# Optimization experiments

Hardware: AMD Instinct MI355X
Metric: run time of the kernel (lower is better)

## Reference

```python
import jax, jax.numpy as jnp
import numpy as np

B, S, H = 2, 2048, 3072
NH, NKV, HD = 32, 8, 96
ROPE_THETA = 10000.0
NEG = -1e9


def setup_inputs() -> dict:
    key = jax.random.key(0)
    k0, k1, k2 = jax.random.split(key, 3)
    hidden_states = jax.random.normal(k0, (B, S, H), jnp.float32) * 0.02
    # rotary embeddings (precomputed, as HF passes position_embeddings=(cos,sin))
    inv_freq = 1.0 / (ROPE_THETA ** (jnp.arange(0, HD, 2, dtype=jnp.float32) / HD))
    pos = jnp.arange(S, dtype=jnp.float32)
    freqs = pos[:, None] * inv_freq[None, :]            # [S, HD/2]
    emb = jnp.concatenate([freqs, freqs], axis=-1)      # [S, HD]
    cos = jnp.broadcast_to(jnp.cos(emb)[None], (B, S, HD))
    sin = jnp.broadcast_to(jnp.sin(emb)[None], (B, S, HD))
    # additive causal mask [B,1,S,S]
    causal = jnp.tril(jnp.ones((S, S), dtype=bool))
    attention_mask = jnp.where(causal, 0.0, NEG).astype(jnp.float32)
    attention_mask = jnp.broadcast_to(attention_mask[None, None], (B, 1, S, S))
    Wqkv = jax.random.normal(k1, ((NH + 2 * NKV) * HD, H), jnp.float32) * 0.02
    Wo = jax.random.normal(k2, (H, NH * HD), jnp.float32) * 0.02
    cache_position = jnp.arange(S, dtype=jnp.int32)
    position_ids = jnp.broadcast_to(jnp.arange(S, dtype=jnp.int32)[None], (B, S))
    return {"hidden_states": hidden_states, "cos": cos, "sin": sin,
            "attention_mask": attention_mask, "Wqkv": Wqkv, "Wo": Wo,
            "cache_position": cache_position, "position_ids": position_ids}


def _rotate_half(x):
    x1, x2 = x[..., : HD // 2], x[..., HD // 2:]
    return jnp.concatenate([-x2, x1], axis=-1)


def reference(hidden_states, cos, sin, attention_mask, Wqkv, Wo, cache_position, position_ids):
    # fused qkv projection (no bias in Phi3)
    qkv = jnp.einsum('bsh,dh->bsd', hidden_states, Wqkv)  # [B,S,(NH+2*NKV)*HD]
    q = qkv[..., : NH * HD].reshape(B, S, NH, HD).transpose(0, 2, 1, 3)           # [B,NH,S,HD]
    k = qkv[..., NH * HD: (NH + NKV) * HD].reshape(B, S, NKV, HD).transpose(0, 2, 1, 3)
    v = qkv[..., (NH + NKV) * HD:].reshape(B, S, NKV, HD).transpose(0, 2, 1, 3)   # [B,NKV,S,HD]
    # rotary embedding (unsqueeze head dim)
    cosb, sinb = cos[:, None], sin[:, None]              # [B,1,S,HD]
    q = q * cosb + _rotate_half(q) * sinb
    k = k * cosb + _rotate_half(k) * sinb
    # DynamicCache() is empty -> cache update is identity (k, v unchanged)
    # GQA: repeat kv heads
    rep = NH // NKV
    k = jnp.repeat(k, rep, axis=1)                       # [B,NH,S,HD]
    v = jnp.repeat(v, rep, axis=1)
    # SDPA
    scale = 1.0 / jnp.sqrt(jnp.float32(HD))
    scores = jnp.einsum('bhqd,bhkd->bhqk', q, k) * scale + attention_mask
    attn = jax.nn.softmax(scores, axis=-1)
    ctx = jnp.einsum('bhqk,bhkd->bhqd', attn, v)         # [B,NH,S,HD]
    ctx = ctx.transpose(0, 2, 1, 3).reshape(B, S, NH * HD)
    out = jnp.einsum('bsd,hd->bsh', ctx, Wo)             # o_proj
    return out
```

## Files before the change

### kernel.cpp

```cpp
#include <hip/hip_runtime.h>

typedef __attribute__((ext_vector_type(8))) __bf16 bf16x8;
typedef __attribute__((ext_vector_type(4))) float f32x4;
typedef __attribute__((ext_vector_type(4))) unsigned int u32x4;
typedef __attribute__((ext_vector_type(4))) unsigned short u16x4;
typedef __attribute__((ext_vector_type(8))) unsigned short u16x8;

__device__ __forceinline__ unsigned short f2bf(float x) {
  unsigned u = __builtin_bit_cast(unsigned, x);
  u += 0x7fffu + ((u >> 16) & 1u);
  return (unsigned short)(u >> 16);
}
__device__ __forceinline__ float bf2f(unsigned short h) {
  unsigned u = ((unsigned)h) << 16;
  return __builtin_bit_cast(float, u);
}
__device__ __forceinline__ bf16x8 ld_frag(const unsigned short* p) {
  u32x4 u = *(const u32x4*)p;
  return __builtin_bit_cast(bf16x8, u);
}
__device__ __forceinline__ void gload_lds16(const unsigned short* g, unsigned short* l) {
  __builtin_amdgcn_global_load_lds(
      (const __attribute__((address_space(1))) void*)g,
      (__attribute__((address_space(3))) void*)l, 16, 0, 0);
}

__global__ __launch_bounds__(256) void cvt_bf16(const float* __restrict__ in,
                                                unsigned short* __restrict__ out, int n4) {
  int i = blockIdx.x * 256 + threadIdx.x;
  if (i >= n4) return;
  f32x4 v = *((const f32x4*)in + i);
  u16x4 o;
  #pragma unroll
  for (int j = 0; j < 4; ++j) o[j] = f2bf(v[j]);
  *((u16x4*)out + i) = o;
}

template <int WRITE_BF16>
__global__ __launch_bounds__(512, 2) void gemm8p(const unsigned short* __restrict__ A,
                                                 const unsigned short* __restrict__ B,
                                                 void* __restrict__ Cv,
                                                 int M, int N, int K) {
  __shared__ __align__(16) unsigned short SM[57344];
  const int nwg = gridDim.x;
  const int swz = (blockIdx.x & 7) * (nwg >> 3) + (blockIdx.x >> 3);
  const int bx = swz & 15, by = swz >> 4;
  const int row0 = bx * 256, col0 = by * 192;
  const int tid = threadIdx.x;
  const int wave = tid >> 6, lane = tid & 63;
  const int g = lane >> 4, r = lane & 15;
  const int wm = (wave >> 2) * 128, wn = (wave & 3) * 48;
  const int NT = K >> 6;

  const unsigned short* Agb = A + (size_t)row0 * K;
  const unsigned short* Bgb = B + (size_t)col0 * K;

  f32x4 acc[8][3] = {};

  auto SU = [&](const unsigned short* src, unsigned short* dst, int u) {
    const int pos = u * 512 + tid;
    const int rw = pos >> 3, cc = pos & 7;
    gload_lds16(src + (size_t)rw * K + ((cc ^ (rw & 7)) * 8), dst + pos * 8);
  };
  auto LDA = [&](const unsigned short* base, int mi, int dk) {
    const int rw = wm + mi * 16 + r;
    return ld_frag(base + rw * 64 + (((dk * 4 + g) ^ (r & 7)) * 8));
  };
  auto LDB = [&](const unsigned short* base, int ni, int dk) {
    const int rw = wn + ni * 16 + r;
    return ld_frag(base + rw * 64 + (((dk * 4 + g) ^ (r & 7)) * 8));
  };

  SU(Agb, SM, 0); SU(Agb, SM, 1); SU(Agb, SM, 2); SU(Agb, SM, 3);
  SU(Bgb, SM + 16384, 0); SU(Bgb, SM + 16384, 1); SU(Bgb, SM + 16384, 2);
  __syncthreads();

  for (int t = 0; t < NT; ++t) {
    const int d = t & 1;
    const unsigned short* Ab = SM + d * 28672;
    const unsigned short* Bb = Ab + 16384;
    unsigned short* An = SM + (d ^ 1) * 28672;
    unsigned short* Bn = An + 16384;
    const unsigned short* Asrc = Agb + (t + 1) * 64;
    const unsigned short* Bsrc = Bgb + (t + 1) * 64;
    const bool pf = (t + 1 < NT);

    bf16x8 a[4], b0, b1, b2;

    b0 = LDB(Bb, 0, 0); b1 = LDB(Bb, 1, 0); b2 = LDB(Bb, 2, 0);
    a[0] = LDA(Ab, 0, 0); a[1] = LDA(Ab, 1, 0); a[2] = LDA(Ab, 2, 0); a[3] = LDA(Ab, 3, 0);
    if (pf) { SU(Asrc, An, 0); SU(Asrc, An, 1); SU(Asrc, An, 2); }
    __builtin_amdgcn_s_barrier();
    asm volatile("s_waitcnt lgkmcnt(0)" ::: "memory");
    __builtin_amdgcn_sched_barrier(0);
    __builtin_amdgcn_s_setprio(1);
    #pragma unroll
    for (int i = 0; i < 4; ++i) {
      acc[i][0] = __builtin_amdgcn_mfma_f32_16x16x32_bf16(a[i], b0, acc[i][0], 0, 0, 0);
      acc[i][1] = __builtin_amdgcn_mfma_f32_16x16x32_bf16(a[i], b1, acc[i][1], 0, 0, 0);
      acc[i][2] = __builtin_amdgcn_mfma_f32_16x16x32_bf16(a[i], b2, acc[i][2], 0, 0, 0);
    }
    __builtin_amdgcn_s_setprio(0);
    __builtin_amdgcn_s_barrier();

    a[0] = LDA(Ab, 4, 0); a[1] = LDA(Ab, 5, 0); a[2] = LDA(Ab, 6, 0); a[3] = LDA(Ab, 7, 0);
    if (pf) { SU(Asrc, An, 3); SU(Bsrc, Bn, 0); }
    __builtin_amdgcn_s_barrier();
    asm volatile("s_waitcnt lgkmcnt(0)" ::: "memory");
    __builtin_amdgcn_sched_barrier(0);
    __builtin_amdgcn_s_setprio(1);
    #pragma unroll
    for (int i = 0; i < 4; ++i) {
      acc[4 + i][0] = __builtin_amdgcn_mfma_f32_16x16x32_bf16(a[i], b0, acc[4 + i][0], 0, 0, 0);
      acc[4 + i][1] = __builtin_amdgcn_mfma_f32_16x16x32_bf16(a[i], b1, acc[4 + i][1], 0, 0, 0);
      acc[4 + i][2] = __builtin_amdgcn_mfma_f32_16x16x32_bf16(a[i], b2, acc[4 + i][2], 0, 0, 0);
    }
    __builtin_amdgcn_s_setprio(0);
    __builtin_amdgcn_s_barrier();

    b0 = LDB(Bb, 0, 1); b1 = LDB(Bb, 1, 1); b2 = LDB(Bb, 2, 1);
    a[0] = LDA(Ab, 0, 1); a[1] = LDA(Ab, 1, 1); a[2] = LDA(Ab, 2, 1); a[3] = LDA(Ab, 3, 1);
    if (pf) { SU(Bsrc, Bn, 1); SU(Bsrc, Bn, 2); }
    __builtin_amdgcn_s_barrier();
    asm volatile("s_waitcnt lgkmcnt(0)" ::: "memory");
    __builtin_amdgcn_sched_barrier(0);
    __builtin_amdgcn_s_setprio(1);
    #pragma unroll
    for (int i = 0; i < 4; ++i) {
      acc[i][0] = __builtin_amdgcn_mfma_f32_16x16x32_bf16(a[i], b0, acc[i][0], 0, 0, 0);
      acc[i][1] = __builtin_amdgcn_mfma_f32_16x16x32_bf16(a[i], b1, acc[i][1], 0, 0, 0);
      acc[i][2] = __builtin_amdgcn_mfma_f32_16x16x32_bf16(a[i], b2, acc[i][2], 0, 0, 0);
    }
    __builtin_amdgcn_s_setprio(0);
    __builtin_amdgcn_s_barrier();

    a[0] = LDA(Ab, 4, 1); a[1] = LDA(Ab, 5, 1); a[2] = LDA(Ab, 6, 1); a[3] = LDA(Ab, 7, 1);
    __builtin_amdgcn_s_barrier();
    asm volatile("s_waitcnt lgkmcnt(0)" ::: "memory");
    __builtin_amdgcn_sched_barrier(0);
    __builtin_amdgcn_s_setprio(1);
    #pragma unroll
    for (int i = 0; i < 4; ++i) {
      acc[4 + i][0] = __builtin_amdgcn_mfma_f32_16x16x32_bf16(a[i], b0, acc[4 + i][0], 0, 0, 0);
      acc[4 + i][1] = __builtin_amdgcn_mfma_f32_16x16x32_bf16(a[i], b1, acc[4 + i][1], 0, 0, 0);
      acc[4 + i][2] = __builtin_amdgcn_mfma_f32_16x16x32_bf16(a[i], b2, acc[4 + i][2], 0, 0, 0);
    }
    __builtin_amdgcn_s_setprio(0);
    asm volatile("s_waitcnt vmcnt(0)" ::: "memory");
    __builtin_amdgcn_s_barrier();
  }

  #pragma unroll
  for (int mi = 0; mi < 8; ++mi)
    #pragma unroll
    for (int n = 0; n < 3; ++n)
      #pragma unroll
      for (int rr = 0; rr < 4; ++rr) {
        const size_t idx = (size_t)(row0 + wm + mi * 16 + g * 4 + rr) * (size_t)N
                         + (col0 + wn + n * 16 + r);
        if (WRITE_BF16) ((unsigned short*)Cv)[idx] = f2bf(acc[mi][n][rr]);
        else            ((float*)Cv)[idx] = acc[mi][n][rr];
      }
}

__global__ __launch_bounds__(256) void rope_qk(unsigned short* __restrict__ qkv,
                                               const float* __restrict__ cs,
                                               const float* __restrict__ sn) {
  const int t = blockIdx.x * 256 + threadIdx.x;
  const int d4 = t % 12;
  const int rest = t / 12;
  const int head = rest % 40;
  const int row = rest / 40;
  const size_t base = (size_t)row * 4608 + head * 96 + d4 * 4;
  const u16x4 a = *(const u16x4*)&qkv[base];
  const u16x4 bq = *(const u16x4*)&qkv[base + 48];
  const int cb = row * 96 + d4 * 4;
  const f32x4 c1 = *(const f32x4*)&cs[cb];
  const f32x4 s1 = *(const f32x4*)&sn[cb];
  const f32x4 c2 = *(const f32x4*)&cs[cb + 48];
  const f32x4 s2 = *(const f32x4*)&sn[cb + 48];
  u16x4 o1, o2;
  #pragma unroll
  for (int j = 0; j < 4; ++j) {
    const float x1 = bf2f(a[j]), x2 = bf2f(bq[j]);
    o1[j] = f2bf(x1 * c1[j] - x2 * s1[j]);
    o2[j] = f2bf(x2 * c2[j] + x1 * s2[j]);
  }
  *(u16x4*)&qkv[base] = o1;
  *(u16x4*)&qkv[base + 48] = o2;
}

__global__ __launch_bounds__(256) void vtrans(const unsigned short* __restrict__ qkv,
                                              unsigned short* __restrict__ vt) {
  __shared__ __align__(16) unsigned short T[64 * 104];
  const int s0 = blockIdx.x * 64;
  const int kvh = blockIdx.y, b = blockIdx.z;
  const int tid = threadIdx.x;
  #pragma unroll
  for (int it = 0; it < 3; ++it) {
    const int c = it * 256 + tid;
    const int sr = c / 12, d0 = (c % 12) * 8;
    *(u32x4*)&T[sr * 104 + d0] =
        *(const u32x4*)&qkv[(size_t)(b * 2048 + s0 + sr) * 4608 + 3840 + kvh * 96 + d0];
  }
  __syncthreads();
  #pragma unroll
  for (int it = 0; it < 3; ++it) {
    const int c = it * 256 + tid;
    const int dr = c >> 3, k0 = (c & 7) * 8;
    u16x8 o;
    #pragma unroll
    for (int j = 0; j < 8; ++j) o[j] = T[(k0 + j) * 104 + dr];
    *(u16x8*)&vt[((size_t)(b * 8 + kvh) * 96 + dr) * 2048 + s0 + k0] = o;
  }
}

__global__ __launch_bounds__(512) void attn_fwd(const unsigned short* __restrict__ qkv,
                                                const unsigned short* __restrict__ vt,
                                                unsigned short* __restrict__ ctx) {
  __shared__ __align__(16) unsigned short SMEM[40960];
  const int wg = blockIdx.x;
  const int xcd = wg & 7, j = wg >> 3;
  const int c = xcd + ((j >> 4) << 3);
  const int b = c >> 3, kvh = c & 7;
  const int rj = j & 15;
  const int h = kvh * 4 + (rj >> 2);
  const int pr = rj & 3;
  const int tid = threadIdx.x;
  const int wave = tid >> 6, lane = tid & 63;
  const int g = lane >> 4, r = lane & 15;
  const float kLS = 0.14724445f;

  const unsigned short* kgbase = qkv + (size_t)(b * 2048) * 4608 + 3072 + kvh * 96;
  const unsigned short* vgbase = vt + (size_t)(b * 8 + kvh) * 96 * 2048;

  auto STAGE = [&](int t, int bi) {
    const int kv0 = t * 64;
    unsigned short* kd = SMEM + bi * 6144;
    unsigned short* vd = SMEM + 12288 + bi * 6144;
    #pragma unroll
    for (int i = 0; i < 3; ++i) {
      const int l = i * 512 + tid;
      if (l < 768) {
        const int dk = l >> 8, rem = l & 255;
        const int row = rem >> 2, cc = rem & 3;
        const int csrc = cc ^ ((row >> 1) & 3);
        gload_lds16(kgbase + (size_t)(kv0 + row) * 4608 + dk * 32 + csrc * 8, kd + l * 8);
      } else {
        const int lv = l - 768;
        const int row = lv >> 3, cc = lv & 7;
        const int csrc = cc ^ (row & 7);
        gload_lds16(vgbase + (size_t)row * 2048 + kv0 + csrc * 8, vd + lv * 8);
      }
    }
  };

  #pragma unroll 1
  for (int sel = 0; sel < 2; ++sel) {
    const int qt = sel ? pr : 7 - pr;
    const int nt = qt * 4 + 4;
    const int q0 = qt * 256 + wave * 32;

    __syncthreads();

    bf16x8 qf[2][3];
    #pragma unroll
    for (int qb = 0; qb < 2; ++qb)
      #pragma unroll
      for (int dk = 0; dk < 3; ++dk)
        qf[qb][dk] = ld_frag(&qkv[(size_t)(b * 2048 + q0 + qb * 16 + r) * 4608 + h * 96 + dk * 32 + g * 8]);

    f32x4 o[6][2] = {};
    float m_[2] = {-1e30f, -1e30f};
    float l_[2] = {0.f, 0.f};

    STAGE(0, 0);
    __syncthreads();

    for (int t = 0; t < nt; ++t) {
      const int cur = t & 1;
      if (t + 1 < nt) STAGE(t + 1, cur ^ 1);
      const int kv0 = t * 64;
      const unsigned short* Ks = SMEM + cur * 6144;
      const unsigned short* Vs = SMEM + 12288 + cur * 6144;
      unsigned short* Ps = SMEM + 24576 + wave * 2048;

      if (kv0 <= q0 + 31) {
        f32x4 st[4][2] = {};
        #pragma unroll
        for (int dk = 0; dk < 3; ++dk) {
          bf16x8 af[4];
          #pragma unroll
          for (int kb = 0; kb < 4; ++kb)
            af[kb] = ld_frag(&Ks[dk * 2048 + (kb * 16 + r) * 32 + ((g ^ ((r >> 1) & 3)) * 8)]);
          __builtin_amdgcn_s_setprio(1);
          #pragma unroll
          for (int kb = 0; kb < 4; ++kb)
            #pragma unroll
            for (int qb = 0; qb < 2; ++qb)
              st[kb][qb] = __builtin_amdgcn_mfma_f32_16x16x32_bf16(af[kb], qf[qb][dk], st[kb][qb], 0, 0, 0);
          __builtin_amdgcn_s_setprio(0);
        }
        if (kv0 + 63 > q0) {
          #pragma unroll
          for (int kb = 0; kb < 4; ++kb)
            #pragma unroll
            for (int qb = 0; qb < 2; ++qb)
              #pragma unroll
              for (int rr = 0; rr < 4; ++rr) {
                const int ka = kv0 + kb * 16 + g * 4 + rr;
                const int qa = q0 + qb * 16 + r;
                const float s = st[kb][qb][rr] * kLS;
                st[kb][qb][rr] = (ka <= qa) ? s : -1e30f;
              }
        } else {
          #pragma unroll
          for (int kb = 0; kb < 4; ++kb)
            #pragma unroll
            for (int qb = 0; qb < 2; ++qb)
              #pragma unroll
              for (int rr = 0; rr < 4; ++rr)
                st[kb][qb][rr] *= kLS;
        }
        #pragma unroll
        for (int qb = 0; qb < 2; ++qb) {
          float mx = st[0][qb][0];
          #pragma unroll
          for (int kb = 0; kb < 4; ++kb)
            #pragma unroll
            for (int rr = 0; rr < 4; ++rr) mx = fmaxf(mx, st[kb][qb][rr]);
          mx = fmaxf(mx, __shfl_xor(mx, 16));
          mx = fmaxf(mx, __shfl_xor(mx, 32));
          if (__all(mx <= m_[qb])) {
            float rs = 0.f;
            #pragma unroll
            for (int kb = 0; kb < 4; ++kb)
              #pragma unroll
              for (int rr = 0; rr < 4; ++rr) {
                const float p = __builtin_amdgcn_exp2f(st[kb][qb][rr] - m_[qb]);
                st[kb][qb][rr] = p;
                rs += p;
              }
            rs += __shfl_xor(rs, 16);
            rs += __shfl_xor(rs, 32);
            l_[qb] += rs;
          } else {
            const float mnew = fmaxf(m_[qb], mx);
            const float corr = __builtin_amdgcn_exp2f(m_[qb] - mnew);
            m_[qb] = mnew;
            float rs = 0.f;
            #pragma unroll
            for (int kb = 0; kb < 4; ++kb)
              #pragma unroll
              for (int rr = 0; rr < 4; ++rr) {
                const float p = __builtin_amdgcn_exp2f(st[kb][qb][rr] - mnew);
                st[kb][qb][rr] = p;
                rs += p;
              }
            rs += __shfl_xor(rs, 16);
            rs += __shfl_xor(rs, 32);
            l_[qb] = l_[qb] * corr + rs;
            #pragma unroll
            for (int db = 0; db < 6; ++db) o[db][qb] *= corr;
          }
        }
        #pragma unroll
        for (int kb = 0; kb < 4; ++kb)
          #pragma unroll
          for (int qb = 0; qb < 2; ++qb) {
            u16x4 w;
            #pragma unroll
            for (int rr = 0; rr < 4; ++rr) w[rr] = f2bf(st[kb][qb][rr]);
            const int q = qb * 16 + r;
            *(u16x4*)&Ps[q * 64 + (((2 * kb + (g >> 1)) ^ (r & 7)) << 3) + (g & 1) * 4] = w;
          }
        #pragma unroll
        for (int kk = 0; kk < 2; ++kk) {
          bf16x8 pb[2];
          #pragma unroll
          for (int qb = 0; qb < 2; ++qb)
            pb[qb] = ld_frag(&Ps[(qb * 16 + r) * 64 + ((kk * 4 + g) ^ (r & 7)) * 8]);
          __builtin_amdgcn_s_setprio(1);
          #pragma unroll
          for (int db = 0; db < 6; ++db) {
            const bf16x8 va = ld_frag(&Vs[(db * 16 + r) * 64 + ((kk * 4 + g) ^ (r & 7)) * 8]);
            #pragma unroll
            for (int qb = 0; qb < 2; ++qb)
              o[db][qb] = __builtin_amdgcn_mfma_f32_16x16x32_bf16(va, pb[qb], o[db][qb], 0, 0, 0);
          }
          __builtin_amdgcn_s_setprio(0);
        }
      }
      __syncthreads();
    }

    const float inv_l[2] = {1.f / l_[0], 1.f / l_[1]};
    unsigned short* obuf = SMEM + wave * 3328;
    #pragma unroll
    for (int db = 0; db < 6; ++db)
      #pragma unroll
      for (int qb = 0; qb < 2; ++qb) {
        u16x4 w;
        #pragma unroll
        for (int rr = 0; rr < 4; ++rr) w[rr] = f2bf(o[db][qb][rr] * inv_l[qb]);
        *(u16x4*)&obuf[(qb * 16 + r) * 104 + db * 16 + g * 4] = w;
      }
    #pragma unroll
    for (int it = 0; it < 6; ++it) {
      const int cc = it * 64 + lane;
      const int qr = cc / 12, d0 = (cc % 12) * 8;
      *(u32x4*)&ctx[(size_t)(b * 2048 + q0 + qr) * 3072 + h * 96 + d0] =
          *(const u32x4*)&obuf[qr * 104 + d0];
    }
  }
}

extern "C" void kernel_launch(void* const* d_in, const int* in_sizes, int n_in,
                              void* d_out, int out_size, void* d_ws, size_t ws_size,
                              hipStream_t stream) {
  const float* hs   = (const float*)d_in[0];
  const float* cosp = (const float*)d_in[1];
  const float* sinp = (const float*)d_in[2];
  const float* wqkv = (const float*)d_in[4];
  const float* wo   = (const float*)d_in[5];
  float* out = (float*)d_out;

  unsigned short* qkv = (unsigned short*)d_ws;
  unsigned short* hsb = qkv + 18874368;
  unsigned short* wqb = hsb + 12582912;
  unsigned short* vt  = hsb;
  unsigned short* wob = hsb + 3145728;
  unsigned short* ctx = wqb;

  cvt_bf16<<<12288, 256, 0, stream>>>(hs,   hsb, 3145728);
  cvt_bf16<<<13824, 256, 0, stream>>>(wqkv, wqb, 3538944);
  gemm8p<1><<<384, 512, 0, stream>>>(hsb, wqb, (void*)qkv, 4096, 4608, 3072);
  rope_qk<<<7680, 256, 0, stream>>>(qkv, cosp, sinp);
  vtrans<<<dim3(32, 8, 2), 256, 0, stream>>>(qkv, vt);
  cvt_bf16<<<9216, 256, 0, stream>>>(wo, wob, 2359296);
  attn_fwd<<<256, 512, 0, stream>>>(qkv, vt, ctx);
  gemm8p<0><<<256, 512, 0, stream>>>(ctx, wob, (void*)out, 4096, 3072, 3072);
}
```

Measured before the change: 351.7 us.

## Switch GEMMs to 256x256 tiles with K=32 triple-buffered LDS pipeline

Replaces the 256x192 tile, K=64 double-buffered GEMM with a 256x256 tile, K=32 step, three-stage LDS ring buffer that prefetches two steps ahead with partial vmcnt waits. Larger output tiles raise arithmetic intensity per loaded byte and cut the workgroup count (288 and 192 instead of 384 and 256). The deeper prefetch aims to hide global load latency better. The cost is more accumulator registers, fewer workgroups than the 256 CUs for the output projection, and more barrier overhead per unit of K.

```diff
diff --git a/kernel.cpp b/kernel.cpp
--- a/kernel.cpp
+++ b/kernel.cpp
@@ -37,129 +37,98 @@
 }
 
 template <int WRITE_BF16>
-__global__ __launch_bounds__(512, 2) void gemm8p(const unsigned short* __restrict__ A,
+__global__ __launch_bounds__(512, 2) void gemm3b(const unsigned short* __restrict__ A,
                                                  const unsigned short* __restrict__ B,
                                                  void* __restrict__ Cv,
                                                  int M, int N, int K) {
-  __shared__ __align__(16) unsigned short SM[57344];
+  __shared__ __align__(16) unsigned short SM[49152];
   const int nwg = gridDim.x;
   const int swz = (blockIdx.x & 7) * (nwg >> 3) + (blockIdx.x >> 3);
   const int bx = swz & 15, by = swz >> 4;
-  const int row0 = bx * 256, col0 = by * 192;
+  const int row0 = bx * 256, col0 = by * 256;
   const int tid = threadIdx.x;
   const int wave = tid >> 6, lane = tid & 63;
   const int g = lane >> 4, r = lane & 15;
-  const int wm = (wave >> 2) * 128, wn = (wave & 3) * 48;
-  const int NT = K >> 6;
+  const int wm = (wave >> 2) * 128, wn = (wave & 3) * 64;
+  const int NT = K >> 5;
 
   const unsigned short* Agb = A + (size_t)row0 * K;
   const unsigned short* Bgb = B + (size_t)col0 * K;
 
-  f32x4 acc[8][3] = {};
-
-  auto SU = [&](const unsigned short* src, unsigned short* dst, int u) {
+  f32x4 acc[8][4] = {};
+
+  auto SU = [&](const unsigned short* src, unsigned short* dst, int kt, int u) {
     const int pos = u * 512 + tid;
-    const int rw = pos >> 3, cc = pos & 7;
-    gload_lds16(src + (size_t)rw * K + ((cc ^ (rw & 7)) * 8), dst + pos * 8);
+    const int rw = pos >> 2, cc = pos & 3;
+    gload_lds16(src + (size_t)rw * K + kt * 32 + ((cc ^ ((rw >> 1) & 3)) * 8),
+                dst + pos * 8);
   };
-  auto LDA = [&](const unsigned short* base, int mi, int dk) {
-    const int rw = wm + mi * 16 + r;
-    return ld_frag(base + rw * 64 + (((dk * 4 + g) ^ (r & 7)) * 8));
+  auto LDF = [&](const unsigned short* base, int row) {
+    return ld_frag(base + row * 32 + ((g ^ ((row >> 1) & 3)) * 8));
   };
-  auto LDB = [&](const unsigned short* base, int ni, int dk) {
-    const int rw = wn + ni * 16 + r;
-    return ld_frag(base + rw * 64 + (((dk * 4 + g) ^ (r & 7)) * 8));
-  };
-
-  SU(Agb, SM, 0); SU(Agb, SM, 1); SU(Agb, SM, 2); SU(Agb, SM, 3);
-  SU(Bgb, SM + 16384, 0); SU(Bgb, SM + 16384, 1); SU(Bgb, SM + 16384, 2);
-  __syncthreads();
+
+  SU(Agb, SM,         0, 0); SU(Agb, SM,         0, 1);
+  SU(Bgb, SM + 8192,  0, 0); SU(Bgb, SM + 8192,  0, 1);
+  SU(Agb, SM + 16384, 1, 0); SU(Agb, SM + 16384, 1, 1);
+  SU(Bgb, SM + 24576, 1, 0); SU(Bgb, SM + 24576, 1, 1);
+  asm volatile("s_waitcnt vmcnt(4)" ::: "memory");
+  __builtin_amdgcn_s_barrier();
 
   for (int t = 0; t < NT; ++t) {
-    const int d = t & 1;
-    const unsigned short* Ab = SM + d * 28672;
-    const unsigned short* Bb = Ab + 16384;
-    unsigned short* An = SM + (d ^ 1) * 28672;
-    unsigned short* Bn = An + 16384;
-    const unsigned short* Asrc = Agb + (t + 1) * 64;
-    const unsigned short* Bsrc = Bgb + (t + 1) * 64;
-    const bool pf = (t + 1 < NT);
-
-    bf16x8 a[4], b0, b1, b2;
-
-    b0 = LDB(Bb, 0, 0); b1 = LDB(Bb, 1, 0); b2 = LDB(Bb, 2, 0);
-    a[0] = LDA(Ab, 0, 0); a[1] = LDA(Ab, 1, 0); a[2] = LDA(Ab, 2, 0); a[3] = LDA(Ab, 3, 0);
-    if (pf) { SU(Asrc, An, 0); SU(Asrc, An, 1); SU(Asrc, An, 2); }
+    const int ct = t % 3, st = (t + 2) % 3;
+    const unsigned short* Ab = SM + ct * 16384;
+    const unsigned short* Bb = Ab + 8192;
+    unsigned short* An = SM + st * 16384;
+    unsigned short* Bn = An + 8192;
+    const bool pf = (t + 2 < NT);
+
+    bf16x8 a[4], b[4];
+
+    a[0] = LDF(Ab, wm + r);      a[1] = LDF(Ab, wm + 16 + r);
+    a[2] = LDF(Ab, wm + 32 + r); a[3] = LDF(Ab, wm + 48 + r);
+    b[0] = LDF(Bb, wn + r);      b[1] = LDF(Bb, wn + 16 + r);
+    b[2] = LDF(Bb, wn + 32 + r); b[3] = LDF(Bb, wn + 48 + r);
+    if (pf) { SU(Agb, An, t + 2, 0); SU(Agb, An, t + 2, 1); }
     __builtin_amdgcn_s_barrier();
     asm volatile("s_waitcnt lgkmcnt(0)" ::: "memory");
     __builtin_amdgcn_sched_barrier(0);
     __builtin_amdgcn_s_setprio(1);
     #pragma unroll
-    for (int i = 0; i < 4; ++i) {
-      acc[i][0] = __builtin_amdgcn_mfma_f32_16x16x32_bf16(a[i], b0, acc[i][0], 0, 0, 0);
-      acc[i][1] = __builtin_amdgcn_mfma_f32_16x16x32_bf16(a[i], b1, acc[i][1], 0, 0, 0);
-      acc[i][2] = __builtin_amdgcn_mfma_f32_16x16x32_bf16(a[i], b2, acc[i][2], 0, 0, 0);
-    }
+    for (int mi = 0; mi < 4; ++mi)
+      #pragma unroll
+      for (int ni = 0; ni < 4; ++ni)
+        acc[mi][ni] = __builtin_amdgcn_mfma_f32_16x16x32_bf16(a[mi], b[ni], acc[mi][ni], 0, 0, 0);
     __builtin_amdgcn_s_setprio(0);
     __builtin_amdgcn_s_barrier();
 
-    a[0] = LDA(Ab, 4, 0); a[1] = LDA(Ab, 5, 0); a[2] = LDA(Ab, 6, 0); a[3] = LDA(Ab, 7, 0);
-    if (pf) { SU(Asrc, An, 3); SU(Bsrc, Bn, 0); }
+    a[0] = LDF(Ab, wm + 64 + r); a[1] = LDF(Ab, wm + 80 + r);
+    a[2] = LDF(Ab, wm + 96 + r); a[3] = LDF(Ab, wm + 112 + r);
+    if (pf) { SU(Bgb, Bn, t + 2, 0); SU(Bgb, Bn, t + 2, 1); }
     __builtin_amdgcn_s_barrier();
     asm volatile("s_waitcnt lgkmcnt(0)" ::: "memory");
     __builtin_amdgcn_sched_barrier(0);
     __builtin_amdgcn_s_setprio(1);
     #pragma unroll
-    for (int i = 0; i < 4; ++i) {
-      acc[4 + i][0] = __builtin_amdgcn_mfma_f32_16x16x32_bf16(a[i], b0, acc[4 + i][0], 0, 0, 0);
-      acc[4 + i][1] = __builtin_amdgcn_mfma_f32_16x16x32_bf16(a[i], b1, acc[4 + i][1], 0, 0, 0);
-      acc[4 + i][2] = __builtin_amdgcn_mfma_f32_16x16x32_bf16(a[i], b2, acc[4 + i][2], 0, 0, 0);
-    }
+    for (int mi = 0; mi < 4; ++mi)
+      #pragma unroll
+      for (int ni = 0; ni < 4; ++ni)
+        acc[4 + mi][ni] = __builtin_amdgcn_mfma_f32_16x16x32_bf16(a[mi], b[ni], acc[4 + mi][ni], 0, 0, 0);
     __builtin_amdgcn_s_setprio(0);
-    __builtin_amdgcn_s_barrier();
-
-    b0 = LDB(Bb, 0, 1); b1 = LDB(Bb, 1, 1); b2 = LDB(Bb, 2, 1);
-    a[0] = LDA(Ab, 0, 1); a[1] = LDA(Ab, 1, 1); a[2] = LDA(Ab, 2, 1); a[3] = LDA(Ab, 3, 1);
-    if (pf) { SU(Bsrc, Bn, 1); SU(Bsrc, Bn, 2); }
-    __builtin_amdgcn_s_barrier();
-    asm volatile("s_waitcnt lgkmcnt(0)" ::: "memory");
-    __builtin_amdgcn_sched_barrier(0);
-    __builtin_amdgcn_s_setprio(1);
-    #pragma unroll
-    for (int i = 0; i < 4; ++i) {
-      acc[i][0] = __builtin_amdgcn_mfma_f32_16x16x32_bf16(a[i], b0, acc[i][0], 0, 0, 0);
-      acc[i][1] = __builtin_amdgcn_mfma_f32_16x16x32_bf16(a[i], b1, acc[i][1], 0, 0, 0);
-      acc[i][2] = __builtin_amdgcn_mfma_f32_16x16x32_bf16(a[i], b2, acc[i][2], 0, 0, 0);
-    }
-    __builtin_amdgcn_s_setprio(0);
-    __builtin_amdgcn_s_barrier();
-
-    a[0] = LDA(Ab, 4, 1); a[1] = LDA(Ab, 5, 1); a[2] = LDA(Ab, 6, 1); a[3] = LDA(Ab, 7, 1);
-    __builtin_amdgcn_s_barrier();
-    asm volatile("s_waitcnt lgkmcnt(0)" ::: "memory");
-    __builtin_amdgcn_sched_barrier(0);
-    __builtin_amdgcn_s_setprio(1);
-    #pragma unroll
-    for (int i = 0; i < 4; ++i) {
-      acc[4 + i][0] = __builtin_amdgcn_mfma_f32_16x16x32_bf16(a[i], b0, acc[4 + i][0], 0, 0, 0);
-      acc[4 + i][1] = __builtin_amdgcn_mfma_f32_16x16x32_bf16(a[i], b1, acc[4 + i][1], 0, 0, 0);
-      acc[4 + i][2] = __builtin_amdgcn_mfma_f32_16x16x32_bf16(a[i], b2, acc[4 + i][2], 0, 0, 0);
-    }
-    __builtin_amdgcn_s_setprio(0);
-    asm volatile("s_waitcnt vmcnt(0)" ::: "memory");
+    if (pf) asm volatile("s_waitcnt vmcnt(4)" ::: "memory");
+    else    asm volatile("s_waitcnt vmcnt(0)" ::: "memory");
     __builtin_amdgcn_s_barrier();
   }
 
   #pragma unroll
   for (int mi = 0; mi < 8; ++mi)
     #pragma unroll
-    for (int n = 0; n < 3; ++n)
+    for (int ni = 0; ni < 4; ++ni)
       #pragma unroll
       for (int rr = 0; rr < 4; ++rr) {
         const size_t idx = (size_t)(row0 + wm + mi * 16 + g * 4 + rr) * (size_t)N
-                         + (col0 + wn + n * 16 + r);
-        if (WRITE_BF16) ((unsigned short*)Cv)[idx] = f2bf(acc[mi][n][rr]);
-        else            ((float*)Cv)[idx] = acc[mi][n][rr];
+                         + (col0 + wn + ni * 16 + r);
+        if (WRITE_BF16) ((unsigned short*)Cv)[idx] = f2bf(acc[mi][ni][rr]);
+        else            ((float*)Cv)[idx] = acc[mi][ni][rr];
       }
 }
 
@@ -434,10 +403,10 @@
 
   cvt_bf16<<<12288, 256, 0, stream>>>(hs,   hsb, 3145728);
   cvt_bf16<<<13824, 256, 0, stream>>>(wqkv, wqb, 3538944);
-  gemm8p<1><<<384, 512, 0, stream>>>(hsb, wqb, (void*)qkv, 4096, 4608, 3072);
+  gemm3b<1><<<288, 512, 0, stream>>>(hsb, wqb, (void*)qkv, 4096, 4608, 3072);
   rope_qk<<<7680, 256, 0, stream>>>(qkv, cosp, sinp);
   vtrans<<<dim3(32, 8, 2), 256, 0, stream>>>(qkv, vt);
   cvt_bf16<<<9216, 256, 0, stream>>>(wo, wob, 2359296);
   attn_fwd<<<256, 512, 0, stream>>>(qkv, vt, ctx);
-  gemm8p<0><<<256, 512, 0, stream>>>(ctx, wob, (void*)out, 4096, 3072, 3072);
-}
+  gemm3b<0><<<192, 512, 0, stream>>>(ctx, wob, (void*)out, 4096, 3072, 3072);
+}
```

After: 416.1 us. 18.3% more time.

## Halve attention query tile per block to double grid size

Applied to the files above, without the earlier changes.

The attention kernel now processes 128-query tiles (16 queries per wave) instead of 256-query tiles, doubling the grid to 512 workgroups and remapping the block-to-(batch, kv-head, head, tile) assignment. Per-wave state shrinks to a single 16-row block, which lowers register and LDS use (LDS drops to 64KB) and may allow more resident blocks per CU. The trade-off is that each K/V tile staged in LDS is reused by half as many queries, so K/V global traffic doubles and each MFMA gets less reuse of the loaded K/V fragments.

```diff
diff --git a/kernel.cpp b/kernel.cpp
--- a/kernel.cpp
+++ b/kernel.cpp
@@ -218,14 +218,14 @@
 __global__ __launch_bounds__(512) void attn_fwd(const unsigned short* __restrict__ qkv,
                                                 const unsigned short* __restrict__ vt,
                                                 unsigned short* __restrict__ ctx) {
-  __shared__ __align__(16) unsigned short SMEM[40960];
+  __shared__ __align__(16) unsigned short SMEM[32768];
   const int wg = blockIdx.x;
   const int xcd = wg & 7, j = wg >> 3;
-  const int c = xcd + ((j >> 4) << 3);
+  const int c = xcd + ((j >> 5) << 3);
   const int b = c >> 3, kvh = c & 7;
-  const int rj = j & 15;
-  const int h = kvh * 4 + (rj >> 2);
-  const int pr = rj & 3;
+  const int rj = j & 31;
+  const int h = kvh * 4 + (rj >> 3);
+  const int pr = rj & 7;
   const int tid = threadIdx.x;
   const int wave = tid >> 6, lane = tid & 63;
   const int g = lane >> 4, r = lane & 15;
@@ -257,22 +257,20 @@
 
   #pragma unroll 1
   for (int sel = 0; sel < 2; ++sel) {
-    const int qt = sel ? pr : 7 - pr;
-    const int nt = qt * 4 + 4;
-    const int q0 = qt * 256 + wave * 32;
+    const int qt = sel ? pr : 15 - pr;
+    const int nt = qt * 2 + 2;
+    const int q0 = qt * 128 + wave * 16;
 
     __syncthreads();
 
-    bf16x8 qf[2][3];
-    #pragma unroll
-    for (int qb = 0; qb < 2; ++qb)
-      #pragma unroll
-      for (int dk = 0; dk < 3; ++dk)
-        qf[qb][dk] = ld_frag(&qkv[(size_t)(b * 2048 + q0 + qb * 16 + r) * 4608 + h * 96 + dk * 32 + g * 8]);
-
-    f32x4 o[6][2] = {};
-    float m_[2] = {-1e30f, -1e30f};
-    float l_[2] = {0.f, 0.f};
+    bf16x8 qf[3];
+    #pragma unroll
+    for (int dk = 0; dk < 3; ++dk)
+      qf[dk] = ld_frag(&qkv[(size_t)(b * 2048 + q0 + r) * 4608 + h * 96 + dk * 32 + g * 8]);
+
+    f32x4 o[6] = {};
+    float m_ = -1e30f;
+    float l_ = 0.f;
 
     STAGE(0, 0);
     __syncthreads();
@@ -283,10 +281,10 @@
       const int kv0 = t * 64;
       const unsigned short* Ks = SMEM + cur * 6144;
       const unsigned short* Vs = SMEM + 12288 + cur * 6144;
-      unsigned short* Ps = SMEM + 24576 + wave * 2048;
-
-      if (kv0 <= q0 + 31) {
-        f32x4 st[4][2] = {};
+      unsigned short* Ps = SMEM + 24576 + wave * 1024;
+
+      if (kv0 <= q0 + 15) {
+        f32x4 st[4] = {};
         #pragma unroll
         for (int dk = 0; dk < 3; ++dk) {
           bf16x8 af[4];
@@ -296,97 +294,82 @@
           __builtin_amdgcn_s_setprio(1);
           #pragma unroll
           for (int kb = 0; kb < 4; ++kb)
-            #pragma unroll
-            for (int qb = 0; qb < 2; ++qb)
-              st[kb][qb] = __builtin_amdgcn_mfma_f32_16x16x32_bf16(af[kb], qf[qb][dk], st[kb][qb], 0, 0, 0);
+            st[kb] = __builtin_amdgcn_mfma_f32_16x16x32_bf16(af[kb], qf[dk], st[kb], 0, 0, 0);
           __builtin_amdgcn_s_setprio(0);
         }
         if (kv0 + 63 > q0) {
           #pragma unroll
           for (int kb = 0; kb < 4; ++kb)
             #pragma unroll
-            for (int qb = 0; qb < 2; ++qb)
-              #pragma unroll
-              for (int rr = 0; rr < 4; ++rr) {
-                const int ka = kv0 + kb * 16 + g * 4 + rr;
-                const int qa = q0 + qb * 16 + r;
-                const float s = st[kb][qb][rr] * kLS;
-                st[kb][qb][rr] = (ka <= qa) ? s : -1e30f;
-              }
+            for (int rr = 0; rr < 4; ++rr) {
+              const int ka = kv0 + kb * 16 + g * 4 + rr;
+              const int qa = q0 + r;
+              const float s = st[kb][rr] * kLS;
+              st[kb][rr] = (ka <= qa) ? s : -1e30f;
+            }
         } else {
           #pragma unroll
           for (int kb = 0; kb < 4; ++kb)
             #pragma unroll
-            for (int qb = 0; qb < 2; ++qb)
-              #pragma unroll
-              for (int rr = 0; rr < 4; ++rr)
-                st[kb][qb][rr] *= kLS;
+            for (int rr = 0; rr < 4; ++rr)
+              st[kb][rr] *= kLS;
         }
-        #pragma unroll
-        for (int qb = 0; qb < 2; ++qb) {
-          float mx = st[0][qb][0];
+        {
+          float mx = st[0][0];
           #pragma unroll
           for (int kb = 0; kb < 4; ++kb)
             #pragma unroll
-            for (int rr = 0; rr < 4; ++rr) mx = fmaxf(mx, st[kb][qb][rr]);
+            for (int rr = 0; rr < 4; ++rr) mx = fmaxf(mx, st[kb][rr]);
           mx = fmaxf(mx, __shfl_xor(mx, 16));
           mx = fmaxf(mx, __shfl_xor(mx, 32));
-          if (__all(mx <= m_[qb])) {
+          if (__all(mx <= m_)) {
             float rs = 0.f;
             #pragma unroll
             for (int kb = 0; kb < 4; ++kb)
               #pragma unroll
               for (int rr = 0; rr < 4; ++rr) {
-                const float p = __builtin_amdgcn_exp2f(st[kb][qb][rr] - m_[qb]);
-                st[kb][qb][rr] = p;
+                const float p = __builtin_amdgcn_exp2f(st[kb][rr] - m_);
+                st[kb][rr] = p;
                 rs += p;
               }
             rs += __shfl_xor(rs, 16);
             rs += __shfl_xor(rs, 32);
-            l_[qb] += rs;
+            l_ += rs;
           } else {
-            const float mnew = fmaxf(m_[qb], mx);
-            const float corr = __builtin_amdgcn_exp2f(m_[qb] - mnew);
-            m_[qb] = mnew;
+            const float mnew = fmaxf(m_, mx);
+            const float corr = __builtin_amdgcn_exp2f(m_ - mnew);
+            m_ = mnew;
             float rs = 0.f;
             #pragma unroll
             for (int kb = 0; kb < 4; ++kb)
               #pragma unroll
               for (int rr = 0; rr < 4; ++rr) {
-                const float p = __builtin_amdgcn_exp2f(st[kb][qb][rr] - mnew);
-                st[kb][qb][rr] = p;
+                const float p = __builtin_amdgcn_exp2f(st[kb][rr] - mnew);
+                st[kb][rr] = p;
                 rs += p;
               }
             rs += __shfl_xor(rs, 16);
             rs += __shfl_xor(rs, 32);
-            l_[qb] = l_[qb] * corr + rs;
-            #pragma unroll
-            for (int db = 0; db < 6; ++db) o[db][qb] *= corr;
+            l_ = l_ * corr + rs;
+            #pragma unroll
+            for (int db = 0; db < 6; ++db) o[db] *= corr;
           }
         }
         #pragma unroll
-        for (int kb = 0; kb < 4; ++kb)
-          #pragma unroll
-          for (int qb = 0; qb < 2; ++qb) {
-            u16x4 w;
-            #pragma unroll
-            for (int rr = 0; rr < 4; ++rr) w[rr] = f2bf(st[kb][qb][rr]);
-            const int q = qb * 16 + r;
-            *(u16x4*)&Ps[q * 64 + (((2 * kb + (g >> 1)) ^ (r & 7)) << 3) + (g & 1) * 4] = w;
-          }
+        for (int kb = 0; kb < 4; ++kb) {
+          u16x4 w;
+          #pragma unroll
+          for (int rr = 0; rr < 4; ++rr) w[rr] = f2bf(st[kb][rr]);
+          *(u16x4*)&Ps[r * 64 + (((2 * kb + (g >> 1)) ^ (r & 7)) << 3) + (g & 1) * 4] = w;
+        }
         #pragma unroll
         for (int kk = 0; kk < 2; ++kk) {
-          bf16x8 pb[2];
-          #pragma unroll
-          for (int qb = 0; qb < 2; ++qb)
-            pb[qb] = ld_frag(&Ps[(qb * 16 + r) * 64 + ((kk * 4 + g) ^ (r & 7)) * 8]);
+          const bf16x8 pb = ld_frag(&Ps[r * 64 + ((kk * 4 + g) ^ (r & 7)) * 8]);
           __builtin_amdgcn_s_setprio(1);
           #pragma unroll
           for (int db = 0; db < 6; ++db) {
             const bf16x8 va = ld_frag(&Vs[(db * 16 + r) * 64 + ((kk * 4 + g) ^ (r & 7)) * 8]);
-            #pragma unroll
-            for (int qb = 0; qb < 2; ++qb)
-              o[db][qb] = __builtin_amdgcn_mfma_f32_16x16x32_bf16(va, pb[qb], o[db][qb], 0, 0, 0);
+            o[db] = __builtin_amdgcn_mfma_f32_16x16x32_bf16(va, pb, o[db], 0, 0, 0);
           }
           __builtin_amdgcn_s_setprio(0);
         }
@@ -394,22 +377,20 @@
       __syncthreads();
     }
 
-    const float inv_l[2] = {1.f / l_[0], 1.f / l_[1]};
-    unsigned short* obuf = SMEM + wave * 3328;
-    #pragma unroll
-    for (int db = 0; db < 6; ++db)
+    const float inv_l = 1.f / l_;
+    unsigned short* obuf = SMEM + wave * 1664;
+    #pragma unroll
+    for (int db = 0; db < 6; ++db) {
+      u16x4 w;
       #pragma unroll
-      for (int qb = 0; qb < 2; ++qb) {
-        u16x4 w;
-        #pragma unroll
-        for (int rr = 0; rr < 4; ++rr) w[rr] = f2bf(o[db][qb][rr] * inv_l[qb]);
-        *(u16x4*)&obuf[(qb * 16 + r) * 104 + db * 16 + g * 4] = w;
-      }
-    #pragma unroll
-    for (int it = 0; it < 6; ++it) {
+      for (int rr = 0; rr < 4; ++rr) w[rr] = f2bf(o[db][rr] * inv_l);
+      *(u16x4*)&obuf[r * 104 + db * 16 + g * 4] = w;
+    }
+    #pragma unroll
+    for (int it = 0; it < 3; ++it) {
       const int cc = it * 64 + lane;
       const int qr = cc / 12, d0 = (cc % 12) * 8;
-      *(u32x4*)&ctx[(size_t)(b * 2048 + q0 + qr) * 3072 + h * 96 + d0] =
+      *(u32x4*)&ctx[(size_t)(b * 2048 + qt * 128 + wave * 16 + qr) * 3072 + h * 96 + d0] =
           *(const u32x4*)&obuf[qr * 104 + d0];
     }
   }
@@ -438,6 +419,6 @@
   rope_qk<<<7680, 256, 0, stream>>>(qkv, cosp, sinp);
   vtrans<<<dim3(32, 8, 2), 256, 0, stream>>>(qkv, vt);
   cvt_bf16<<<9216, 256, 0, stream>>>(wo, wob, 2359296);
-  attn_fwd<<<256, 512, 0, stream>>>(qkv, vt, ctx);
+  attn_fwd<<<512, 512, 0, stream>>>(qkv, vt, ctx);
   gemm8p<0><<<256, 512, 0, stream>>>(ctx, wob, (void*)out, 4096, 3072, 3072);
 }
```

New measurement: 367.8 us. +4.6%, slower.

## Fuse RoPE into QKV GEMM epilogue with per-wave 64x96 head-aligned tiles

Applied to the files above, without the earlier changes.

The GEMM wave tiling changes from 128x48 to 64x96, so each wave's column span covers exactly one 96-wide head. That lets the QKV GEMM epilogue apply rotary embedding to the q and k columns directly, pairing accumulators n and n+3 (d and d+48), and the separate rope_qk kernel is removed. This saves one read-modify-write pass over the q/k part of qkv and one launch. In exchange the new wave shape does more LDS B-fragment loads per A fragment, and the epilogue now reads cos/sin with scalar loads.

```diff
diff --git a/kernel.cpp b/kernel.cpp
--- a/kernel.cpp
+++ b/kernel.cpp
@@ -36,10 +36,12 @@
   *((u16x4*)out + i) = o;
 }
 
-template <int WRITE_BF16>
+template <int MODE>
 __global__ __launch_bounds__(512, 2) void gemm8p(const unsigned short* __restrict__ A,
                                                  const unsigned short* __restrict__ B,
                                                  void* __restrict__ Cv,
+                                                 const float* __restrict__ cs,
+                                                 const float* __restrict__ sn,
                                                  int M, int N, int K) {
   __shared__ __align__(16) unsigned short SM[57344];
   const int nwg = gridDim.x;
@@ -49,13 +51,13 @@
   const int tid = threadIdx.x;
   const int wave = tid >> 6, lane = tid & 63;
   const int g = lane >> 4, r = lane & 15;
-  const int wm = (wave >> 2) * 128, wn = (wave & 3) * 48;
+  const int wm = (wave >> 1) * 64, wn = (wave & 1) * 96;
   const int NT = K >> 6;
 
   const unsigned short* Agb = A + (size_t)row0 * K;
   const unsigned short* Bgb = B + (size_t)col0 * K;
 
-  f32x4 acc[8][3] = {};
+  f32x4 acc[4][6] = {};
 
   auto SU = [&](const unsigned short* src, unsigned short* dst, int u) {
     const int pos = u * 512 + tid;
@@ -85,109 +87,115 @@
     const unsigned short* Bsrc = Bgb + (t + 1) * 64;
     const bool pf = (t + 1 < NT);
 
-    bf16x8 a[4], b0, b1, b2;
-
-    b0 = LDB(Bb, 0, 0); b1 = LDB(Bb, 1, 0); b2 = LDB(Bb, 2, 0);
-    a[0] = LDA(Ab, 0, 0); a[1] = LDA(Ab, 1, 0); a[2] = LDA(Ab, 2, 0); a[3] = LDA(Ab, 3, 0);
+    bf16x8 a0, a1, b[6];
+
+    b[0] = LDB(Bb, 0, 0); b[1] = LDB(Bb, 1, 0); b[2] = LDB(Bb, 2, 0);
+    b[3] = LDB(Bb, 3, 0); b[4] = LDB(Bb, 4, 0); b[5] = LDB(Bb, 5, 0);
+    a0 = LDA(Ab, 0, 0); a1 = LDA(Ab, 1, 0);
     if (pf) { SU(Asrc, An, 0); SU(Asrc, An, 1); SU(Asrc, An, 2); }
     __builtin_amdgcn_s_barrier();
     asm volatile("s_waitcnt lgkmcnt(0)" ::: "memory");
     __builtin_amdgcn_sched_barrier(0);
     __builtin_amdgcn_s_setprio(1);
     #pragma unroll
-    for (int i = 0; i < 4; ++i) {
-      acc[i][0] = __builtin_amdgcn_mfma_f32_16x16x32_bf16(a[i], b0, acc[i][0], 0, 0, 0);
-      acc[i][1] = __builtin_amdgcn_mfma_f32_16x16x32_bf16(a[i], b1, acc[i][1], 0, 0, 0);
-      acc[i][2] = __builtin_amdgcn_mfma_f32_16x16x32_bf16(a[i], b2, acc[i][2], 0, 0, 0);
+    for (int n = 0; n < 6; ++n) {
+      acc[0][n] = __builtin_amdgcn_mfma_f32_16x16x32_bf16(a0, b[n], acc[0][n], 0, 0, 0);
+      acc[1][n] = __builtin_amdgcn_mfma_f32_16x16x32_bf16(a1, b[n], acc[1][n], 0, 0, 0);
     }
     __builtin_amdgcn_s_setprio(0);
     __builtin_amdgcn_s_barrier();
 
-    a[0] = LDA(Ab, 4, 0); a[1] = LDA(Ab, 5, 0); a[2] = LDA(Ab, 6, 0); a[3] = LDA(Ab, 7, 0);
+    a0 = LDA(Ab, 2, 0); a1 = LDA(Ab, 3, 0);
     if (pf) { SU(Asrc, An, 3); SU(Bsrc, Bn, 0); }
     __builtin_amdgcn_s_barrier();
     asm volatile("s_waitcnt lgkmcnt(0)" ::: "memory");
     __builtin_amdgcn_sched_barrier(0);
     __builtin_amdgcn_s_setprio(1);
     #pragma unroll
-    for (int i = 0; i < 4; ++i) {
-      acc[4 + i][0] = __builtin_amdgcn_mfma_f32_16x16x32_bf16(a[i], b0, acc[4 + i][0], 0, 0, 0);
-      acc[4 + i][1] = __builtin_amdgcn_mfma_f32_16x16x32_bf16(a[i], b1, acc[4 + i][1], 0, 0, 0);
-      acc[4 + i][2] = __builtin_amdgcn_mfma_f32_16x16x32_bf16(a[i], b2, acc[4 + i][2], 0, 0, 0);
+    for (int n = 0; n < 6; ++n) {
+      acc[2][n] = __builtin_amdgcn_mfma_f32_16x16x32_bf16(a0, b[n], acc[2][n], 0, 0, 0);
+      acc[3][n] = __builtin_amdgcn_mfma_f32_16x16x32_bf16(a1, b[n], acc[3][n], 0, 0, 0);
     }
     __builtin_amdgcn_s_setprio(0);
     __builtin_amdgcn_s_barrier();
 
-    b0 = LDB(Bb, 0, 1); b1 = LDB(Bb, 1, 1); b2 = LDB(Bb, 2, 1);
-    a[0] = LDA(Ab, 0, 1); a[1] = LDA(Ab, 1, 1); a[2] = LDA(Ab, 2, 1); a[3] = LDA(Ab, 3, 1);
+    b[0] = LDB(Bb, 0, 1); b[1] = LDB(Bb, 1, 1); b[2] = LDB(Bb, 2, 1);
+    b[3] = LDB(Bb, 3, 1); b[4] = LDB(Bb, 4, 1); b[5] = LDB(Bb, 5, 1);
+    a0 = LDA(Ab, 0, 1); a1 = LDA(Ab, 1, 1);
     if (pf) { SU(Bsrc, Bn, 1); SU(Bsrc, Bn, 2); }
     __builtin_amdgcn_s_barrier();
     asm volatile("s_waitcnt lgkmcnt(0)" ::: "memory");
     __builtin_amdgcn_sched_barrier(0);
     __builtin_amdgcn_s_setprio(1);
     #pragma unroll
-    for (int i = 0; i < 4; ++i) {
-      acc[i][0] = __builtin_amdgcn_mfma_f32_16x16x32_bf16(a[i], b0, acc[i][0], 0, 0, 0);
-      acc[i][1] = __builtin_amdgcn_mfma_f32_16x16x32_bf16(a[i], b1, acc[i][1], 0, 0, 0);
-      acc[i][2] = __builtin_amdgcn_mfma_f32_16x16x32_bf16(a[i], b2, acc[i][2], 0, 0, 0);
+    for (int n = 0; n < 6; ++n) {
+      acc[0][n] = __builtin_amdgcn_mfma_f32_16x16x32_bf16(a0, b[n], acc[0][n], 0, 0, 0);
+      acc[1][n] = __builtin_amdgcn_mfma_f32_16x16x32_bf16(a1, b[n], acc[1][n], 0, 0, 0);
     }
     __builtin_amdgcn_s_setprio(0);
     __builtin_amdgcn_s_barrier();
 
-    a[0] = LDA(Ab, 4, 1); a[1] = LDA(Ab, 5, 1); a[2] = LDA(Ab, 6, 1); a[3] = LDA(Ab, 7, 1);
+    a0 = LDA(Ab, 2, 1); a1 = LDA(Ab, 3, 1);
     __builtin_amdgcn_s_barrier();
     asm volatile("s_waitcnt lgkmcnt(0)" ::: "memory");
     __builtin_amdgcn_sched_barrier(0);
     __builtin_amdgcn_s_setprio(1);
     #pragma unroll
-    for (int i = 0; i < 4; ++i) {
-      acc[4 + i][0] = __builtin_amdgcn_mfma_f32_16x16x32_bf16(a[i], b0, acc[4 + i][0], 0, 0, 0);
-      acc[4 + i][1] = __builtin_amdgcn_mfma_f32_16x16x32_bf16(a[i], b1, acc[4 + i][1], 0, 0, 0);
-      acc[4 + i][2] = __builtin_amdgcn_mfma_f32_16x16x32_bf16(a[i], b2, acc[4 + i][2], 0, 0, 0);
+    for (int n = 0; n < 6; ++n) {
+      acc[2][n] = __builtin_amdgcn_mfma_f32_16x16x32_bf16(a0, b[n], acc[2][n], 0, 0, 0);
+      acc[3][n] = __builtin_amdgcn_mfma_f32_16x16x32_bf16(a1, b[n], acc[3][n], 0, 0, 0);
     }
     __builtin_amdgcn_s_setprio(0);
     asm volatile("s_waitcnt vmcnt(0)" ::: "memory");
     __builtin_amdgcn_s_barrier();
   }
 
-  #pragma unroll
-  for (int mi = 0; mi < 8; ++mi)
-    #pragma unroll
-    for (int n = 0; n < 3; ++n)
+  if (MODE == 0) {
+    float* outp = (float*)Cv;
+    #pragma unroll
+    for (int mi = 0; mi < 4; ++mi)
       #pragma unroll
-      for (int rr = 0; rr < 4; ++rr) {
-        const size_t idx = (size_t)(row0 + wm + mi * 16 + g * 4 + rr) * (size_t)N
-                         + (col0 + wn + n * 16 + r);
-        if (WRITE_BF16) ((unsigned short*)Cv)[idx] = f2bf(acc[mi][n][rr]);
-        else            ((float*)Cv)[idx] = acc[mi][n][rr];
-      }
-}
-
-__global__ __launch_bounds__(256) void rope_qk(unsigned short* __restrict__ qkv,
-                                               const float* __restrict__ cs,
-                                               const float* __restrict__ sn) {
-  const int t = blockIdx.x * 256 + threadIdx.x;
-  const int d4 = t % 12;
-  const int rest = t / 12;
-  const int head = rest % 40;
-  const int row = rest / 40;
-  const size_t base = (size_t)row * 4608 + head * 96 + d4 * 4;
-  const u16x4 a = *(const u16x4*)&qkv[base];
-  const u16x4 bq = *(const u16x4*)&qkv[base + 48];
-  const int cb = row * 96 + d4 * 4;
-  const f32x4 c1 = *(const f32x4*)&cs[cb];
-  const f32x4 s1 = *(const f32x4*)&sn[cb];
-  const f32x4 c2 = *(const f32x4*)&cs[cb + 48];
-  const f32x4 s2 = *(const f32x4*)&sn[cb + 48];
-  u16x4 o1, o2;
-  #pragma unroll
-  for (int j = 0; j < 4; ++j) {
-    const float x1 = bf2f(a[j]), x2 = bf2f(bq[j]);
-    o1[j] = f2bf(x1 * c1[j] - x2 * s1[j]);
-    o2[j] = f2bf(x2 * c2[j] + x1 * s2[j]);
+      for (int n = 0; n < 6; ++n)
+        #pragma unroll
+        for (int rr = 0; rr < 4; ++rr) {
+          const size_t idx = (size_t)(row0 + wm + mi * 16 + g * 4 + rr) * (size_t)N
+                           + (col0 + wn + n * 16 + r);
+          outp[idx] = acc[mi][n][rr];
+        }
+  } else {
+    unsigned short* outp = (unsigned short*)Cv;
+    const int hc0 = col0 + wn;
+    if (hc0 < 3840) {
+      #pragma unroll
+      for (int mi = 0; mi < 4; ++mi)
+        #pragma unroll
+        for (int rr = 0; rr < 4; ++rr) {
+          const int row = row0 + wm + mi * 16 + g * 4 + rr;
+          const int cb = row * 96;
+          const size_t rb = (size_t)row * N + hc0;
+          #pragma unroll
+          for (int n = 0; n < 3; ++n) {
+            const int d = n * 16 + r;
+            const float x1 = acc[mi][n][rr], x2 = acc[mi][n + 3][rr];
+            const float c1 = cs[cb + d], s1 = sn[cb + d];
+            const float c2 = cs[cb + d + 48], s2 = sn[cb + d + 48];
+            outp[rb + d]      = f2bf(x1 * c1 - x2 * s1);
+            outp[rb + d + 48] = f2bf(x2 * c2 + x1 * s2);
+          }
+        }
+    } else {
+      #pragma unroll
+      for (int mi = 0; mi < 4; ++mi)
+        #pragma unroll
+        for (int n = 0; n < 6; ++n)
+          #pragma unroll
+          for (int rr = 0; rr < 4; ++rr) {
+            const size_t idx = (size_t)(row0 + wm + mi * 16 + g * 4 + rr) * (size_t)N
+                             + (col0 + wn + n * 16 + r);
+            outp[idx] = f2bf(acc[mi][n][rr]);
+          }
+    }
   }
-  *(u16x4*)&qkv[base] = o1;
-  *(u16x4*)&qkv[base + 48] = o2;
 }
 
 __global__ __launch_bounds__(256) void vtrans(const unsigned short* __restrict__ qkv,
@@ -434,10 +442,9 @@
 
   cvt_bf16<<<12288, 256, 0, stream>>>(hs,   hsb, 3145728);
   cvt_bf16<<<13824, 256, 0, stream>>>(wqkv, wqb, 3538944);
-  gemm8p<1><<<384, 512, 0, stream>>>(hsb, wqb, (void*)qkv, 4096, 4608, 3072);
-  rope_qk<<<7680, 256, 0, stream>>>(qkv, cosp, sinp);
+  gemm8p<1><<<384, 512, 0, stream>>>(hsb, wqb, (void*)qkv, cosp, sinp, 4096, 4608, 3072);
   vtrans<<<dim3(32, 8, 2), 256, 0, stream>>>(qkv, vt);
   cvt_bf16<<<9216, 256, 0, stream>>>(wo, wob, 2359296);
   attn_fwd<<<256, 512, 0, stream>>>(qkv, vt, ctx);
-  gemm8p<0><<<256, 512, 0, stream>>>(ctx, wob, (void*)out, 4096, 3072, 3072);
-}
+  gemm8p<0><<<256, 512, 0, stream>>>(ctx, wob, (void*)out, cosp, sinp, 4096, 3072, 3072);
+}
```

New measurement: 342.3 us. 1.03x faster.
